# Kernel optimization log

Hardware: AMD Instinct MI355X
Metric: run time of the kernel (lower is better)

The kernel has to match this reference:

```python
import jax, jax.numpy as jnp
import numpy as np

# -------- problem dimensions (match init_kwargs / input_specs) --------
B, N, D = 4, 16384, 64          # batch, nodes (=128*128 pixels), feature dim
Q = 128                         # plateau/propagation state width (hardcoded in forward)
W = H = 128                     # grid (hardcoded in forward)
E = 131072                      # edges per batch element
M = 4                           # num_masks = k_nodes - 1
NUM_ITERS = 25                  # GraphPropagator(num_iters=25)
ADJ_THRESH = 0.5                # GraphPropagator(adj_thresh=0.5)


def setup_inputs() -> dict:
    key = jax.random.key(0)
    k1, k2, k3, k4 = jax.random.split(key, 4)
    node_features = jax.random.normal(k1, (B, N, D), dtype=jnp.float32)
    # global node indices in [0, B*N) -- the torch code concatenates per-batch
    # edge lists directly into a (B*N, B*N) SparseTensor
    node_edges = jax.random.randint(k2, (B, 2, E), 0, B * N)
    node_weights = jax.random.uniform(k3, (B, E), dtype=jnp.float32)
    init_state = jax.random.normal(k4, (B, N, Q), dtype=jnp.float32)
    return {"node_features": node_features, "node_edges": node_edges,
            "node_weights": node_weights, "init_state": init_state}


def _propagate(init_state, rows, cols, ws):
    """25-iteration sparse label propagation on the global (B*N,B*N) graph."""
    h = init_state.reshape(B * N, Q)

    def step(h, _):
        msg = ws[:, None] * h[cols]                                  # gather  [B*E, Q]
        agg = jax.ops.segment_sum(msg, rows, num_segments=B * N)    # scatter [B*N, Q]
        hn = agg / (jnp.linalg.norm(agg, axis=-1, keepdims=True) + 1e-8)
        return hn, None

    h, _ = jax.lax.scan(step, h, None, length=NUM_ITERS)
    return h  # [B*N, Q]


def _competition(platmap):
    """Competition(num_masks=M): agents claim pixels by plateau-vector affinity;
    an extra zero-logit background channel yields the unharvested mask."""
    flat = platmap.reshape(B, W * H, Q)
    agent_idx = jnp.linspace(0, W * H - 1, M).astype(jnp.int32)      # deterministic agent pixels
    agents = flat[:, agent_idx, :]                                   # [B, M, Q]
    logits = jnp.einsum('bnq,bmq->bnm', flat, agents) / jnp.sqrt(jnp.float32(Q))
    logits_ext = jnp.concatenate([logits, jnp.zeros((B, W * H, 1), logits.dtype)], axis=-1)
    probs = jax.nn.softmax(logits_ext, axis=-1)                      # [B, WH, M+1]
    masks = probs[..., :M].reshape(B, W, H, M)
    unharv = probs[..., M:].reshape(B, W, H, 1)
    alive = jnp.ones((B, M, 1), dtype=platmap.dtype)
    pheno = agents
    return masks, agents, alive, pheno, unharv


def reference(node_features, node_edges, node_weights, init_state):
    rows = node_edges[:, 0, :].reshape(-1)                           # [B*E] global row idx
    cols = node_edges[:, 1, :].reshape(-1)
    ws = node_weights.reshape(-1)
    ws = jnp.where(ws > ADJ_THRESH, ws, jnp.float32(0.0))            # adjacency threshold

    prop = _propagate(init_state, rows, cols, ws)                    # [B*N, Q]
    platmap = prop.reshape(B, W, H, Q)

    masks, agents, alive, pheno, unharv = _competition(platmap)
    masks_ext = jnp.concatenate([masks, unharv], axis=-1)            # [B, W, H, M+1]
    masks_ext = jnp.transpose(masks_ext, (0, 3, 1, 2))               # [B, M+1, W, H]

    nf = jnp.einsum('bnd,bmn->bmd', node_features,
                    masks_ext.reshape(B, M + 1, W * H))              # [B, M+1, D]
    # F.normalize(p=2, dim=1, eps=1e-12)
    nf = nf / jnp.clip(jnp.linalg.norm(nf, axis=1, keepdims=True), 1e-12)
    node_scores = jnp.max(masks_ext, axis=(-1, -2))                  # [B, M+1]
    return nf, masks_ext, node_scores
```

## Files before the change

### kernel.cpp

```cpp
#include <hip/hip_runtime.h>

#define B_    4
#define N_    16384
#define D_    64
#define Q_    128
#define E_    131072
#define M_    4
#define BN    65536
#define TOTE  524288
#define ITERS 25
#define PAD_CAP (TOTE + 3 * BN + 64)

#define OFF_MASKS 1280
#define OFF_SCORES 328960

__constant__ int c_agidx[4] = {0, 5461, 10922, 16383};

__device__ __forceinline__ unsigned pack_bf16x2(float x, float y) {
    unsigned ux = __float_as_uint(x);
    unsigned uy = __float_as_uint(y);
    ux = (ux + 0x7fffu + ((ux >> 16) & 1u)) >> 16;
    uy = (uy + 0x7fffu + ((uy >> 16) & 1u)) & 0xffff0000u;
    return ux | uy;
}

__global__ void k_count(const int* __restrict__ edges, const float* __restrict__ wts,
                        int* __restrict__ deg) {
    int idx = blockIdx.x * blockDim.x + threadIdx.x;
    if (idx >= TOTE) return;
    int b = idx >> 17;
    int e = idx & (E_ - 1);
    float w = wts[idx];
    if (w > 0.5f) {
        int row = edges[(b * 2) * E_ + e];
        atomicAdd(&deg[row], 1);
    }
}

__global__ __launch_bounds__(256) void k_scan1(const int* __restrict__ deg,
                                               int* __restrict__ blockSums) {
    int i = blockIdx.x * 256 + threadIdx.x;
    int v = (deg[i] + 3) & ~3;
    #pragma unroll
    for (int off = 1; off < 64; off <<= 1) v += __shfl_xor(v, off, 64);
    __shared__ int ws[4];
    int lane = threadIdx.x & 63, w = threadIdx.x >> 6;
    if (lane == 0) ws[w] = v;
    __syncthreads();
    if (threadIdx.x == 0)
        blockSums[blockIdx.x] = ws[0] + ws[1] + ws[2] + ws[3];
}

__global__ __launch_bounds__(256) void k_scan3(const int* __restrict__ deg,
                                               const int* __restrict__ blockSums,
                                               int* __restrict__ row_start,
                                               int* __restrict__ cursor) {
    int t = threadIdx.x;
    int lane = t & 63, w = t >> 6;
    __shared__ int offs[256];
    __shared__ int wtotA[4];
    __shared__ int wtotB[4];

    int bs = blockSums[t];
    int binc = bs;
    #pragma unroll
    for (int off = 1; off < 64; off <<= 1) {
        int u = __shfl_up(binc, off, 64);
        if (lane >= off) binc += u;
    }
    if (lane == 63) wtotA[w] = binc;
    __syncthreads();
    int badd = 0;
    for (int j = 0; j < w; ++j) badd += wtotA[j];
    offs[t] = binc + badd - bs;
    if (blockIdx.x == 0 && t == 255) row_start[BN] = binc + badd;
    __syncthreads();
    int blockOff = offs[blockIdx.x];

    int i = blockIdx.x * 256 + t;
    int v = (deg[i] + 3) & ~3;
    int incl = v;
    #pragma unroll
    for (int off = 1; off < 64; off <<= 1) {
        int u = __shfl_up(incl, off, 64);
        if (lane >= off) incl += u;
    }
    if (lane == 63) wtotB[w] = incl;
    __syncthreads();
    int wadd = 0;
    for (int j = 0; j < w; ++j) wadd += wtotB[j];
    int rs = blockOff + wadd + incl - v;
    row_start[i] = rs;
    cursor[i] = rs;
}

__global__ void k_scatter(const int* __restrict__ edges, const float* __restrict__ wts,
                          int* __restrict__ cursor, int2* __restrict__ cw) {
    int idx = blockIdx.x * blockDim.x + threadIdx.x;
    if (idx >= TOTE) return;
    int b = idx >> 17;
    int e = idx & (E_ - 1);
    float w = wts[idx];
    if (w > 0.5f) {
        int row = edges[(b * 2) * E_ + e];
        int col = edges[(b * 2) * E_ + E_ + e];
        int pos = atomicAdd(&cursor[row], 1);
        cw[pos] = make_int2(col, __float_as_int(w));
    }
}

__global__ void k_sort(const int* __restrict__ row_start, const int* __restrict__ deg,
                       int2* __restrict__ cw) {
    int n = blockIdx.x * blockDim.x + threadIdx.x;
    if (n >= BN) return;
    int s = row_start[n], epos = s + deg[n], pend = row_start[n + 1];
    for (int i = s + 1; i < epos; ++i) {
        int2 v = cw[i];
        unsigned long long key =
            ((unsigned long long)(unsigned)v.x << 32) | (unsigned)v.y;
        int j = i - 1;
        while (j >= s) {
            int2 u = cw[j];
            unsigned long long kj =
                ((unsigned long long)(unsigned)u.x << 32) | (unsigned)u.y;
            if (kj <= key) break;
            cw[j + 1] = u;
            --j;
        }
        cw[j + 1] = v;
    }
    for (int i = epos; i < pend; ++i) cw[i] = make_int2(0, 0);
}

template <bool F32IN>
__global__ __launch_bounds__(256) void k_prop(const void* __restrict__ hin,
                                              unsigned* __restrict__ hout,
                                              const int* __restrict__ row_start,
                                              const int2* __restrict__ cw) {
    int lane = threadIdx.x & 63;
    int wid = (blockIdx.x << 2) + (threadIdx.x >> 6);

    auto gather = [&](int col) -> float2 {
        if constexpr (F32IN) {
            return ((const float2*)hin)[((size_t)col << 6) + lane];
        } else {
            unsigned p = ((const unsigned*)hin)[((size_t)col << 6) + lane];
            float2 r;
            r.x = __uint_as_float(p << 16);
            r.y = __uint_as_float(p & 0xffff0000u);
            return r;
        }
    };

    #pragma unroll 1
    for (int k = 0; k < 4; ++k) {
        int gid = wid + (k << 13);
        int uA = __builtin_amdgcn_readfirstlane(gid);
        int uB = uA + 32768;
        int sA = row_start[uA], eA = row_start[uA + 1];
        int sB = row_start[uB], eB = row_start[uB + 1];
        int cA = (eA - sA) >> 2, cB = (eB - sB) >> 2;
        int nmax = cA > cB ? cA : cB;
        int baseA = cA ? sA : sB;
        int baseB = cB ? sB : sA;
        int lastA = (cA ? cA : 1) - 1;
        int lastB = (cB ? cB : 1) - 1;

        float axA = 0.f, ayA = 0.f, axB = 0.f, ayB = 0.f;
        for (int j = 0; j < nmax; ++j) {
            int jA = j < lastA ? j : lastA;
            int jB = j < lastB ? j : lastB;
            const int4* qA = (const int4*)(cw + baseA + (jA << 2));
            const int4* qB = (const int4*)(cw + baseB + (jB << 2));
            int4 a0 = qA[0], a1 = qA[1];
            int4 b0 = qB[0], b1 = qB[1];
            float2 vA0 = gather(a0.x);
            float2 vA1 = gather(a0.z);
            float2 vA2 = gather(a1.x);
            float2 vA3 = gather(a1.z);
            float2 vB0 = gather(b0.x);
            float2 vB1 = gather(b0.z);
            float2 vB2 = gather(b1.x);
            float2 vB3 = gather(b1.z);
            bool okA = j < cA, okB = j < cB;
            float wA0 = okA ? __int_as_float(a0.y) : 0.f;
            float wA1 = okA ? __int_as_float(a0.w) : 0.f;
            float wA2 = okA ? __int_as_float(a1.y) : 0.f;
            float wA3 = okA ? __int_as_float(a1.w) : 0.f;
            float wB0 = okB ? __int_as_float(b0.y) : 0.f;
            float wB1 = okB ? __int_as_float(b0.w) : 0.f;
            float wB2 = okB ? __int_as_float(b1.y) : 0.f;
            float wB3 = okB ? __int_as_float(b1.w) : 0.f;
            axA = fmaf(wA0, vA0.x, axA); ayA = fmaf(wA0, vA0.y, ayA);
            axA = fmaf(wA1, vA1.x, axA); ayA = fmaf(wA1, vA1.y, ayA);
            axA = fmaf(wA2, vA2.x, axA); ayA = fmaf(wA2, vA2.y, ayA);
            axA = fmaf(wA3, vA3.x, axA); ayA = fmaf(wA3, vA3.y, ayA);
            axB = fmaf(wB0, vB0.x, axB); ayB = fmaf(wB0, vB0.y, ayB);
            axB = fmaf(wB1, vB1.x, axB); ayB = fmaf(wB1, vB1.y, ayB);
            axB = fmaf(wB2, vB2.x, axB); ayB = fmaf(wB2, vB2.y, ayB);
            axB = fmaf(wB3, vB3.x, axB); ayB = fmaf(wB3, vB3.y, ayB);
        }
        float ssA = axA * axA + ayA * ayA;
        float ssB = axB * axB + ayB * ayB;
        #pragma unroll
        for (int off = 32; off; off >>= 1) {
            ssA += __shfl_xor(ssA, off, 64);
            ssB += __shfl_xor(ssB, off, 64);
        }
        float invA = 1.0f / (sqrtf(ssA) + 1e-8f);
        float invB = 1.0f / (sqrtf(ssB) + 1e-8f);
        hout[((size_t)uA << 6) + lane] = pack_bf16x2(axA * invA, ayA * invA);
        hout[((size_t)uB << 6) + lane] = pack_bf16x2(axB * invB, ayB * invB);
    }
}

__global__ __launch_bounds__(256) void k_masks(const unsigned* __restrict__ h,
                                               float* __restrict__ masks) {
    int wave = threadIdx.x >> 6;
    int lane = threadIdx.x & 63;
    int n = blockIdx.x * 4 + wave;
    int b = n >> 14;
    int nl = n & (N_ - 1);
    unsigned vp = h[((size_t)n << 6) + lane];
    float vx = __uint_as_float(vp << 16);
    float vy = __uint_as_float(vp & 0xffff0000u);
    float dot[4];
    #pragma unroll
    for (int m = 0; m < 4; ++m) {
        int an = b * N_ + c_agidx[m];
        unsigned ap = h[((size_t)an << 6) + lane];
        float axx = __uint_as_float(ap << 16);
        float ayy = __uint_as_float(ap & 0xffff0000u);
        float d = vx * axx + vy * ayy;
        #pragma unroll
        for (int off = 32; off; off >>= 1) d += __shfl_xor(d, off, 64);
        dot[m] = d;
    }
    const float scl = 0.0883883476483184405501055452631f;
    float l0 = dot[0] * scl, l1 = dot[1] * scl, l2 = dot[2] * scl, l3 = dot[3] * scl;
    float mx = fmaxf(fmaxf(fmaxf(l0, l1), fmaxf(l2, l3)), 0.f);
    float e0 = expf(l0 - mx), e1 = expf(l1 - mx), e2 = expf(l2 - mx),
          e3 = expf(l3 - mx), e4 = expf(0.f - mx);
    float den = e0 + e1 + e2 + e3 + e4;
    if (lane < 5) {
        float p = (lane == 0) ? e0 : (lane == 1) ? e1 : (lane == 2) ? e2
                  : (lane == 3) ? e3 : e4;
        masks[((size_t)b * 5 + lane) * N_ + nl] = p / den;
    }
}

__global__ __launch_bounds__(256) void k_nfpart(const float* __restrict__ feat,
                                                const float* __restrict__ masks,
                                                float* __restrict__ part,
                                                float* __restrict__ maxpart) {
    int b = blockIdx.x >> 6;
    int chunk = blockIdx.x & 63;
    int d = threadIdx.x & 63;
    int g = threadIdx.x >> 6;
    int n0 = chunk * 256 + g * 64;
    const float* fb = feat + (size_t)b * N_ * D_;
    float acc[5] = {0.f, 0.f, 0.f, 0.f, 0.f};
    float mxv[5] = {-1e30f, -1e30f, -1e30f, -1e30f, -1e30f};
    for (int i = 0; i < 64; ++i) {
        int n = n0 + i;
        float fv = fb[(size_t)n * D_ + d];
        #pragma unroll
        for (int m = 0; m < 5; ++m) {
            float mv = masks[((size_t)b * 5 + m) * N_ + n];
            acc[m] = fmaf(fv, mv, acc[m]);
            mxv[m] = fmaxf(mxv[m], mv);
        }
    }
    __shared__ float lds[4][5][64];
    __shared__ float lmx[4][5];
    #pragma unroll
    for (int m = 0; m < 5; ++m) lds[g][m][d] = acc[m];
    if (d == 0) {
        #pragma unroll
        for (int m = 0; m < 5; ++m) lmx[g][m] = mxv[m];
    }
    __syncthreads();
    if (g == 0) {
        #pragma unroll
        for (int m = 0; m < 5; ++m) {
            float s = lds[0][m][d] + lds[1][m][d] + lds[2][m][d] + lds[3][m][d];
            part[(((size_t)b * 64 + chunk) * 5 + m) * 64 + d] = s;
            if (d == 0)
                maxpart[((size_t)b * 64 + chunk) * 5 + m] =
                    fmaxf(fmaxf(lmx[0][m], lmx[1][m]), fmaxf(lmx[2][m], lmx[3][m]));
        }
    }
}

__global__ void k_nffinal(const float* __restrict__ part, const float* __restrict__ maxpart,
                          float* __restrict__ out) {
    int b = blockIdx.x;
    int d = threadIdx.x;
    float v[5];
    float ss = 0.f;
    for (int m = 0; m < 5; ++m) {
        float s = 0.f;
        for (int c = 0; c < 64; ++c)
            s += part[(((size_t)b * 64 + c) * 5 + m) * 64 + d];
        v[m] = s;
        ss += s * s;
    }
    float nrm = fmaxf(sqrtf(ss), 1e-12f);
    for (int m = 0; m < 5; ++m) out[((size_t)b * 5 + m) * 64 + d] = v[m] / nrm;
    if (d < 5) {
        float mx = -1e30f;
        for (int c = 0; c < 64; ++c)
            mx = fmaxf(mx, maxpart[((size_t)b * 64 + c) * 5 + d]);
        out[OFF_SCORES + b * 5 + d] = mx;
    }
}

extern "C" void kernel_launch(void* const* d_in, const int* in_sizes, int n_in,
                              void* d_out, int out_size, void* d_ws, size_t ws_size,
                              hipStream_t stream) {
    const float* feat  = (const float*)d_in[0];
    const int*   edges = (const int*)d_in[1];
    const float* wts   = (const float*)d_in[2];
    const float* init  = (const float*)d_in[3];
    float* out = (float*)d_out;

    unsigned* hA = (unsigned*)d_ws;
    unsigned* hB = hA + (size_t)BN * 64;
    int* row_start  = (int*)(hB + (size_t)BN * 64);
    int* cursor     = row_start + 65544;
    int* deg        = cursor + BN;
    int* blockSums  = deg + BN;
    int2* cw        = (int2*)(blockSums + 256);
    float* part     = (float*)(cw + PAD_CAP);
    float* maxpart  = part + 81920;

    hipMemsetAsync(deg, 0, BN * sizeof(int), stream);
    k_count<<<TOTE / 256, 256, 0, stream>>>(edges, wts, deg);
    k_scan1<<<256, 256, 0, stream>>>(deg, blockSums);
    k_scan3<<<256, 256, 0, stream>>>(deg, blockSums, row_start, cursor);
    k_scatter<<<TOTE / 256, 256, 0, stream>>>(edges, wts, cursor, cw);
    k_sort<<<BN / 256, 256, 0, stream>>>(row_start, deg, cw);

    k_prop<true><<<2048, 256, 0, stream>>>(init, hA, row_start, cw);
    const unsigned* src = hA;
    for (int it = 1; it < ITERS; ++it) {
        unsigned* dst = (it & 1) ? hB : hA;
        k_prop<false><<<2048, 256, 0, stream>>>(src, dst, row_start, cw);
        src = dst;
    }

    k_masks<<<BN / 4, 256, 0, stream>>>(src, out + OFF_MASKS);
    k_nfpart<<<4 * 64, 256, 0, stream>>>(feat, out + OFF_MASKS, part, maxpart);
    k_nffinal<<<4, 64, 0, stream>>>(part, maxpart, out);
}
```

Measured before the change: 535.9 us.

## Fuse mask softmax into feature reduction and give each wave one row pair

k_prop used to loop over four row pairs per wave on 2048 blocks. It now launches BN/8 blocks so each wave handles a single row pair, which gives more parallelism and less serial latency per wave. The separate k_masks and k_nfpart kernels are merged into k_masksnf. It stages the agent vectors in LDS, computes the softmax masks and accumulates the feature-weighted sums in one pass, so the masks are never re-read from global memory and one launch is removed. The fused kernel runs on only 256 blocks, each processing 256 nodes with four shuffle reductions per node, so it may have less parallelism than the old 16384-block masks kernel.

```diff
diff --git a/kernel.cpp b/kernel.cpp
--- a/kernel.cpp
+++ b/kernel.cpp
@@ -138,7 +138,17 @@
                                               const int* __restrict__ row_start,
                                               const int2* __restrict__ cw) {
     int lane = threadIdx.x & 63;
-    int wid = (blockIdx.x << 2) + (threadIdx.x >> 6);
+    int gid = (blockIdx.x << 2) + (threadIdx.x >> 6);
+    int uA = __builtin_amdgcn_readfirstlane(gid);
+    int uB = uA + 32768;
+    int sA = row_start[uA], eA = row_start[uA + 1];
+    int sB = row_start[uB], eB = row_start[uB + 1];
+    int cA = (eA - sA) >> 2, cB = (eB - sB) >> 2;
+    int nmax = cA > cB ? cA : cB;
+    int baseA = cA ? sA : sB;
+    int baseB = cB ? sB : sA;
+    int lastA = (cA ? cA : 1) - 1;
+    int lastB = (cB ? cB : 1) - 1;
 
     auto gather = [&](int col) -> float2 {
         if constexpr (F32IN) {
@@ -152,130 +162,126 @@
         }
     };
 
-    #pragma unroll 1
-    for (int k = 0; k < 4; ++k) {
-        int gid = wid + (k << 13);
-        int uA = __builtin_amdgcn_readfirstlane(gid);
-        int uB = uA + 32768;
-        int sA = row_start[uA], eA = row_start[uA + 1];
-        int sB = row_start[uB], eB = row_start[uB + 1];
-        int cA = (eA - sA) >> 2, cB = (eB - sB) >> 2;
-        int nmax = cA > cB ? cA : cB;
-        int baseA = cA ? sA : sB;
-        int baseB = cB ? sB : sA;
-        int lastA = (cA ? cA : 1) - 1;
-        int lastB = (cB ? cB : 1) - 1;
-
-        float axA = 0.f, ayA = 0.f, axB = 0.f, ayB = 0.f;
-        for (int j = 0; j < nmax; ++j) {
-            int jA = j < lastA ? j : lastA;
-            int jB = j < lastB ? j : lastB;
-            const int4* qA = (const int4*)(cw + baseA + (jA << 2));
-            const int4* qB = (const int4*)(cw + baseB + (jB << 2));
-            int4 a0 = qA[0], a1 = qA[1];
-            int4 b0 = qB[0], b1 = qB[1];
-            float2 vA0 = gather(a0.x);
-            float2 vA1 = gather(a0.z);
-            float2 vA2 = gather(a1.x);
-            float2 vA3 = gather(a1.z);
-            float2 vB0 = gather(b0.x);
-            float2 vB1 = gather(b0.z);
-            float2 vB2 = gather(b1.x);
-            float2 vB3 = gather(b1.z);
-            bool okA = j < cA, okB = j < cB;
-            float wA0 = okA ? __int_as_float(a0.y) : 0.f;
-            float wA1 = okA ? __int_as_float(a0.w) : 0.f;
-            float wA2 = okA ? __int_as_float(a1.y) : 0.f;
-            float wA3 = okA ? __int_as_float(a1.w) : 0.f;
-            float wB0 = okB ? __int_as_float(b0.y) : 0.f;
-            float wB1 = okB ? __int_as_float(b0.w) : 0.f;
-            float wB2 = okB ? __int_as_float(b1.y) : 0.f;
-            float wB3 = okB ? __int_as_float(b1.w) : 0.f;
-            axA = fmaf(wA0, vA0.x, axA); ayA = fmaf(wA0, vA0.y, ayA);
-            axA = fmaf(wA1, vA1.x, axA); ayA = fmaf(wA1, vA1.y, ayA);
-            axA = fmaf(wA2, vA2.x, axA); ayA = fmaf(wA2, vA2.y, ayA);
-            axA = fmaf(wA3, vA3.x, axA); ayA = fmaf(wA3, vA3.y, ayA);
-            axB = fmaf(wB0, vB0.x, axB); ayB = fmaf(wB0, vB0.y, ayB);
-            axB = fmaf(wB1, vB1.x, axB); ayB = fmaf(wB1, vB1.y, ayB);
-            axB = fmaf(wB2, vB2.x, axB); ayB = fmaf(wB2, vB2.y, ayB);
-            axB = fmaf(wB3, vB3.x, axB); ayB = fmaf(wB3, vB3.y, ayB);
-        }
-        float ssA = axA * axA + ayA * ayA;
-        float ssB = axB * axB + ayB * ayB;
+    float axA = 0.f, ayA = 0.f, axB = 0.f, ayB = 0.f;
+    for (int j = 0; j < nmax; ++j) {
+        int jA = j < lastA ? j : lastA;
+        int jB = j < lastB ? j : lastB;
+        const int4* qA = (const int4*)(cw + baseA + (jA << 2));
+        const int4* qB = (const int4*)(cw + baseB + (jB << 2));
+        int4 a0 = qA[0], a1 = qA[1];
+        int4 b0 = qB[0], b1 = qB[1];
+        float2 vA0 = gather(a0.x);
+        float2 vA1 = gather(a0.z);
+        float2 vA2 = gather(a1.x);
+        float2 vA3 = gather(a1.z);
+        float2 vB0 = gather(b0.x);
+        float2 vB1 = gather(b0.z);
+        float2 vB2 = gather(b1.x);
+        float2 vB3 = gather(b1.z);
+        bool okA = j < cA, okB = j < cB;
+        float wA0 = okA ? __int_as_float(a0.y) : 0.f;
+        float wA1 = okA ? __int_as_float(a0.w) : 0.f;
+        float wA2 = okA ? __int_as_float(a1.y) : 0.f;
+        float wA3 = okA ? __int_as_float(a1.w) : 0.f;
+        float wB0 = okB ? __int_as_float(b0.y) : 0.f;
+        float wB1 = okB ? __int_as_float(b0.w) : 0.f;
+        float wB2 = okB ? __int_as_float(b1.y) : 0.f;
+        float wB3 = okB ? __int_as_float(b1.w) : 0.f;
+        axA = fmaf(wA0, vA0.x, axA); ayA = fmaf(wA0, vA0.y, ayA);
+        axA = fmaf(wA1, vA1.x, axA); ayA = fmaf(wA1, vA1.y, ayA);
+        axA = fmaf(wA2, vA2.x, axA); ayA = fmaf(wA2, vA2.y, ayA);
+        axA = fmaf(wA3, vA3.x, axA); ayA = fmaf(wA3, vA3.y, ayA);
+        axB = fmaf(wB0, vB0.x, axB); ayB = fmaf(wB0, vB0.y, ayB);
+        axB = fmaf(wB1, vB1.x, axB); ayB = fmaf(wB1, vB1.y, ayB);
+        axB = fmaf(wB2, vB2.x, axB); ayB = fmaf(wB2, vB2.y, ayB);
+        axB = fmaf(wB3, vB3.x, axB); ayB = fmaf(wB3, vB3.y, ayB);
+    }
+    float ssA = axA * axA + ayA * ayA;
+    float ssB = axB * axB + ayB * ayB;
+    #pragma unroll
+    for (int off = 32; off; off >>= 1) {
+        ssA += __shfl_xor(ssA, off, 64);
+        ssB += __shfl_xor(ssB, off, 64);
+    }
+    float invA = 1.0f / (sqrtf(ssA) + 1e-8f);
+    float invB = 1.0f / (sqrtf(ssB) + 1e-8f);
+    hout[((size_t)uA << 6) + lane] = pack_bf16x2(axA * invA, ayA * invA);
+    hout[((size_t)uB << 6) + lane] = pack_bf16x2(axB * invB, ayB * invB);
+}
+
+__global__ __launch_bounds__(256) void k_masksnf(const unsigned* __restrict__ h,
+                                                 const float* __restrict__ feat,
+                                                 float* __restrict__ masks,
+                                                 float* __restrict__ part,
+                                                 float* __restrict__ maxpart) {
+    int b = blockIdx.x >> 6;
+    int chunk = blockIdx.x & 63;
+    int g = threadIdx.x >> 6;
+    int lane = threadIdx.x & 63;
+
+    __shared__ unsigned ag[4][64];
+    ag[g][lane] = h[((size_t)(b * N_ + c_agidx[g]) << 6) + lane];
+    __syncthreads();
+    float amx[4], amy[4];
+    #pragma unroll
+    for (int m = 0; m < 4; ++m) {
+        unsigned ap = ag[m][lane];
+        amx[m] = __uint_as_float(ap << 16);
+        amy[m] = __uint_as_float(ap & 0xffff0000u);
+    }
+
+    const float* fb = feat + (size_t)b * N_ * D_;
+    const float scl = 0.0883883476483184405501055452631f;
+    int n0 = chunk * 256 + g * 64;
+    float acc[5] = {0.f, 0.f, 0.f, 0.f, 0.f};
+    float mxv[5] = {-1e30f, -1e30f, -1e30f, -1e30f, -1e30f};
+
+    for (int i = 0; i < 64; ++i) {
+        int n = n0 + i;
+        unsigned vp = h[((size_t)(b * N_ + n) << 6) + lane];
+        float vx = __uint_as_float(vp << 16);
+        float vy = __uint_as_float(vp & 0xffff0000u);
+        float d0 = vx * amx[0] + vy * amy[0];
+        float d1 = vx * amx[1] + vy * amy[1];
+        float d2 = vx * amx[2] + vy * amy[2];
+        float d3 = vx * amx[3] + vy * amy[3];
         #pragma unroll
         for (int off = 32; off; off >>= 1) {
-            ssA += __shfl_xor(ssA, off, 64);
-            ssB += __shfl_xor(ssB, off, 64);
-        }
-        float invA = 1.0f / (sqrtf(ssA) + 1e-8f);
-        float invB = 1.0f / (sqrtf(ssB) + 1e-8f);
-        hout[((size_t)uA << 6) + lane] = pack_bf16x2(axA * invA, ayA * invA);
-        hout[((size_t)uB << 6) + lane] = pack_bf16x2(axB * invB, ayB * invB);
-    }
-}
-
-__global__ __launch_bounds__(256) void k_masks(const unsigned* __restrict__ h,
-                                               float* __restrict__ masks) {
-    int wave = threadIdx.x >> 6;
-    int lane = threadIdx.x & 63;
-    int n = blockIdx.x * 4 + wave;
-    int b = n >> 14;
-    int nl = n & (N_ - 1);
-    unsigned vp = h[((size_t)n << 6) + lane];
-    float vx = __uint_as_float(vp << 16);
-    float vy = __uint_as_float(vp & 0xffff0000u);
-    float dot[4];
-    #pragma unroll
-    for (int m = 0; m < 4; ++m) {
-        int an = b * N_ + c_agidx[m];
-        unsigned ap = h[((size_t)an << 6) + lane];
-        float axx = __uint_as_float(ap << 16);
-        float ayy = __uint_as_float(ap & 0xffff0000u);
-        float d = vx * axx + vy * ayy;
-        #pragma unroll
-        for (int off = 32; off; off >>= 1) d += __shfl_xor(d, off, 64);
-        dot[m] = d;
-    }
-    const float scl = 0.0883883476483184405501055452631f;
-    float l0 = dot[0] * scl, l1 = dot[1] * scl, l2 = dot[2] * scl, l3 = dot[3] * scl;
-    float mx = fmaxf(fmaxf(fmaxf(l0, l1), fmaxf(l2, l3)), 0.f);
-    float e0 = expf(l0 - mx), e1 = expf(l1 - mx), e2 = expf(l2 - mx),
-          e3 = expf(l3 - mx), e4 = expf(0.f - mx);
-    float den = e0 + e1 + e2 + e3 + e4;
-    if (lane < 5) {
-        float p = (lane == 0) ? e0 : (lane == 1) ? e1 : (lane == 2) ? e2
-                  : (lane == 3) ? e3 : e4;
-        masks[((size_t)b * 5 + lane) * N_ + nl] = p / den;
-    }
-}
-
-__global__ __launch_bounds__(256) void k_nfpart(const float* __restrict__ feat,
-                                                const float* __restrict__ masks,
-                                                float* __restrict__ part,
-                                                float* __restrict__ maxpart) {
-    int b = blockIdx.x >> 6;
-    int chunk = blockIdx.x & 63;
-    int d = threadIdx.x & 63;
-    int g = threadIdx.x >> 6;
-    int n0 = chunk * 256 + g * 64;
-    const float* fb = feat + (size_t)b * N_ * D_;
-    float acc[5] = {0.f, 0.f, 0.f, 0.f, 0.f};
-    float mxv[5] = {-1e30f, -1e30f, -1e30f, -1e30f, -1e30f};
-    for (int i = 0; i < 64; ++i) {
-        int n = n0 + i;
-        float fv = fb[(size_t)n * D_ + d];
-        #pragma unroll
-        for (int m = 0; m < 5; ++m) {
-            float mv = masks[((size_t)b * 5 + m) * N_ + n];
-            acc[m] = fmaf(fv, mv, acc[m]);
-            mxv[m] = fmaxf(mxv[m], mv);
-        }
-    }
+            d0 += __shfl_xor(d0, off, 64);
+            d1 += __shfl_xor(d1, off, 64);
+            d2 += __shfl_xor(d2, off, 64);
+            d3 += __shfl_xor(d3, off, 64);
+        }
+        float l0 = d0 * scl, l1 = d1 * scl, l2 = d2 * scl, l3 = d3 * scl;
+        float mx = fmaxf(fmaxf(fmaxf(l0, l1), fmaxf(l2, l3)), 0.f);
+        float e0 = expf(l0 - mx), e1 = expf(l1 - mx), e2 = expf(l2 - mx),
+              e3 = expf(l3 - mx), e4 = expf(0.f - mx);
+        float rden = 1.0f / (e0 + e1 + e2 + e3 + e4);
+        float p0 = e0 * rden, p1 = e1 * rden, p2 = e2 * rden,
+              p3 = e3 * rden, p4 = e4 * rden;
+        if (lane < 5) {
+            float p = (lane == 0) ? p0 : (lane == 1) ? p1 : (lane == 2) ? p2
+                      : (lane == 3) ? p3 : p4;
+            masks[((size_t)b * 5 + lane) * N_ + n] = p;
+        }
+        float fv = fb[(size_t)n * D_ + lane];
+        acc[0] = fmaf(fv, p0, acc[0]);
+        acc[1] = fmaf(fv, p1, acc[1]);
+        acc[2] = fmaf(fv, p2, acc[2]);
+        acc[3] = fmaf(fv, p3, acc[3]);
+        acc[4] = fmaf(fv, p4, acc[4]);
+        mxv[0] = fmaxf(mxv[0], p0);
+        mxv[1] = fmaxf(mxv[1], p1);
+        mxv[2] = fmaxf(mxv[2], p2);
+        mxv[3] = fmaxf(mxv[3], p3);
+        mxv[4] = fmaxf(mxv[4], p4);
+    }
+
     __shared__ float lds[4][5][64];
     __shared__ float lmx[4][5];
     #pragma unroll
-    for (int m = 0; m < 5; ++m) lds[g][m][d] = acc[m];
-    if (d == 0) {
+    for (int m = 0; m < 5; ++m) lds[g][m][lane] = acc[m];
+    if (lane == 0) {
         #pragma unroll
         for (int m = 0; m < 5; ++m) lmx[g][m] = mxv[m];
     }
@@ -283,9 +289,9 @@
     if (g == 0) {
         #pragma unroll
         for (int m = 0; m < 5; ++m) {
-            float s = lds[0][m][d] + lds[1][m][d] + lds[2][m][d] + lds[3][m][d];
-            part[(((size_t)b * 64 + chunk) * 5 + m) * 64 + d] = s;
-            if (d == 0)
+            float s = lds[0][m][lane] + lds[1][m][lane] + lds[2][m][lane] + lds[3][m][lane];
+            part[(((size_t)b * 64 + chunk) * 5 + m) * 64 + lane] = s;
+            if (lane == 0)
                 maxpart[((size_t)b * 64 + chunk) * 5 + m] =
                     fmaxf(fmaxf(lmx[0][m], lmx[1][m]), fmaxf(lmx[2][m], lmx[3][m]));
         }
@@ -341,15 +347,14 @@
     k_scatter<<<TOTE / 256, 256, 0, stream>>>(edges, wts, cursor, cw);
     k_sort<<<BN / 256, 256, 0, stream>>>(row_start, deg, cw);
 
-    k_prop<true><<<2048, 256, 0, stream>>>(init, hA, row_start, cw);
+    k_prop<true><<<BN / 8, 256, 0, stream>>>(init, hA, row_start, cw);
     const unsigned* src = hA;
     for (int it = 1; it < ITERS; ++it) {
         unsigned* dst = (it & 1) ? hB : hA;
-        k_prop<false><<<2048, 256, 0, stream>>>(src, dst, row_start, cw);
+        k_prop<false><<<BN / 8, 256, 0, stream>>>(src, dst, row_start, cw);
         src = dst;
     }
 
-    k_masks<<<BN / 4, 256, 0, stream>>>(src, out + OFF_MASKS);
-    k_nfpart<<<4 * 64, 256, 0, stream>>>(feat, out + OFF_MASKS, part, maxpart);
+    k_masksnf<<<4 * 64, 256, 0, stream>>>(src, feat, out + OFF_MASKS, part, maxpart);
     k_nffinal<<<4, 64, 0, stream>>>(part, maxpart, out);
 }
```

After: 568.4 us. 6.1% more time.
